# Performance work log

Measured on AMD Instinct MI355X. Metric: run time of the kernel, lower is better.

Reference implementation:

```python
import jax, jax.numpy as jnp
import numpy as np

TS = 6      # texture cube size (hard-coded in module)
S = 256     # image size (NMR default / ref image size)
DIST = 2.732


def _look_at(verts, eye):
    # NMR look_at: camera at eye, looking at origin, up=(0,1,0)
    eye = jnp.asarray(eye, verts.dtype)
    z = -eye / jnp.linalg.norm(eye)
    up = jnp.array([0.0, 1.0, 0.0], verts.dtype)
    x = jnp.cross(up, z)
    x = x / jnp.linalg.norm(x)
    y = jnp.cross(z, x)
    R = jnp.stack([x, y, z])          # rows = camera axes
    return (verts - eye) @ R.T


def _render(verts, faces, tex_flat, eye):
    # verts [V,3], faces [F,3] int, tex_flat [F*TS^3, 3] (tanh already applied)
    v = _look_at(verts, eye)
    fv = v[faces]                      # [F,3,3]
    p0, p1, p2 = fv[:, 0], fv[:, 1], fv[:, 2]
    ps = (2.0 * jnp.arange(S, dtype=verts.dtype) + 1.0 - S) / S
    PX = jnp.broadcast_to(ps[None, :], (S, S)).reshape(-1)      # x right
    PY = jnp.broadcast_to(-ps[:, None], (S, S)).reshape(-1)     # y up (row 0 = top)

    def edge(a, b):
        # signed edge function, [F,HW]
        return ((PX[None, :] - a[:, 0:1]) * (b[:, 1:2] - a[:, 1:2])
                - (PY[None, :] - a[:, 1:2]) * (b[:, 0:1] - a[:, 0:1]))

    e0 = edge(p1, p2)
    e1 = edge(p2, p0)
    e2 = edge(p0, p1)
    # per-face signed area (double area) [F,1]
    area = ((p1[:, 0] - p0[:, 0]) * (p2[:, 1] - p0[:, 1])
            - (p1[:, 1] - p0[:, 1]) * (p2[:, 0] - p0[:, 0]))[:, None]
    ok = jnp.abs(area) > 1e-8
    inv = jnp.where(ok, 1.0 / jnp.where(ok, area, 1.0), 0.0)
    w0, w1, w2 = e0 * inv, e1 * inv, e2 * inv            # barycentric weights
    inside = (w0 >= 0) & (w1 >= 0) & (w2 >= 0) & ok       # both windings (fill_back)
    z = w0 * p0[:, 2:3] + w1 * p1[:, 2:3] + w2 * p2[:, 2:3]
    depth = jnp.where(inside & (z > 0), z, jnp.inf)       # z-buffer candidates
    best = jnp.argmin(depth, axis=0)                      # [HW] winning face
    hit = jnp.take_along_axis(depth, best[None, :], axis=0)[0] < jnp.inf
    wb = jnp.stack([jnp.take_along_axis(w, best[None, :], axis=0)[0]
                    for w in (w0, w1, w2)], axis=-1)       # [HW,3]
    ti = jnp.clip(jnp.round(wb * (TS - 1)), 0, TS - 1).astype(jnp.int32)
    flat = ((best * TS + ti[:, 0]) * TS + ti[:, 1]) * TS + ti[:, 2]
    colors = tex_flat[flat]                                # [HW,3] gather
    img = jnp.where(hit[:, None], colors, 0.0)
    return img.reshape(S, S, 3).transpose(2, 0, 1)[None]   # [1,3,S,S]


def setup_inputs() -> dict:
    key = jax.random.key(0)
    k1, k2, k3, k4, k5 = jax.random.split(key, 5)
    V, F = 252, 500
    return {
        "vertices": jax.random.normal(k1, (1, V, 3), jnp.float32),
        "faces": jax.random.randint(k2, (1, F, 3), 0, V, jnp.int64),
        "textures": jax.random.normal(k3, (1, F, TS, TS, TS, 3), jnp.float32),
        "image_ref": jax.random.uniform(k4, (1, 3, S, S), jnp.float32),
        "image_ref_2": jax.random.uniform(k5, (1, 3, S, S), jnp.float32),
    }


def reference(vertices, faces, textures, image_ref, image_ref_2):
    tex_flat = jnp.tanh(textures[0]).reshape(-1, 3)
    v, f = vertices[0], faces[0]
    # eye = get_points_from_angles(2.732, 180, 0) -> (0, 0, +d)
    img1 = _render(v, f, tex_flat, jnp.array([0.0, 0.0, DIST], jnp.float32))
    loss_one_side = jnp.sum((img1 - image_ref) ** 2)
    # eye = get_points_from_angles(2.732, 0, 0) -> (0, 0, -d)
    img2 = _render(v, f, tex_flat, jnp.array([0.0, 0.0, -DIST], jnp.float32))
    loss_symmetric = jnp.sum((img2 - image_ref_2) ** 2)
    return (loss_one_side + loss_symmetric) / 2
```

## Files before the change

kernel.cpp:

```cpp
#include <hip/hip_runtime.h>
#include <math.h>

#define IMG_S 256
#define NPIX (IMG_S * IMG_S)
#define NFACE 500
#define NCHUNK 8
#define FPC 64
#define PPT 8
#define TSZ 6
#define DIST 2.732f

struct FaceCoef {
    float A0, B0, C0, A1, B1, C1, A2, B2, C2, Az, Bz, Cz;
};

__device__ __forceinline__ void edge_coef(float ax, float ay, float bx, float by,
                                          float inv, float& A, float& B, float& C) {
    float dy = by - ay;
    float dx = bx - ax;
    A = dy * inv;
    B = -dx * inv;
    C = (ay * dx - ax * dy) * inv;
}

__device__ __forceinline__ bool compute_face_bbox(const float* __restrict__ verts,
                                                  const int* __restrict__ faces,
                                                  int f, int view, FaceCoef& fc,
                                                  float& ymin, float& ymax, float& zmax) {
    int i0 = faces[f * 3 + 0];
    int i1 = faces[f * 3 + 1];
    int i2 = faces[f * 3 + 2];

    float v0x = verts[i0 * 3 + 0], v0y = verts[i0 * 3 + 1], v0z = verts[i0 * 3 + 2];
    float v1x = verts[i1 * 3 + 0], v1y = verts[i1 * 3 + 1], v1z = verts[i1 * 3 + 2];
    float v2x = verts[i2 * 3 + 0], v2y = verts[i2 * 3 + 1], v2z = verts[i2 * 3 + 2];

    float p0x, p0y, p0z, p1x, p1y, p1z, p2x, p2y, p2z;
    if (view == 0) {
        p0x = -v0x; p0y = v0y; p0z = DIST - v0z;
        p1x = -v1x; p1y = v1y; p1z = DIST - v1z;
        p2x = -v2x; p2y = v2y; p2z = DIST - v2z;
    } else {
        p0x = v0x; p0y = v0y; p0z = v0z + DIST;
        p1x = v1x; p1y = v1y; p1z = v1z + DIST;
        p2x = v2x; p2y = v2y; p2z = v2z + DIST;
    }

    ymin = fminf(p0y, fminf(p1y, p2y));
    ymax = fmaxf(p0y, fmaxf(p1y, p2y));
    zmax = fmaxf(p0z, fmaxf(p1z, p2z));

    float area = (p1x - p0x) * (p2y - p0y) - (p1y - p0y) * (p2x - p0x);
    bool ok = fabsf(area) > 1e-8f;
    if (!ok) return false;

    float inv = 1.0f / area;
    edge_coef(p1x, p1y, p2x, p2y, inv, fc.A0, fc.B0, fc.C0);
    edge_coef(p2x, p2y, p0x, p0y, inv, fc.A1, fc.B1, fc.C1);
    edge_coef(p0x, p0y, p1x, p1y, inv, fc.A2, fc.B2, fc.C2);
    fc.Az = fc.A0 * p0z + fc.A1 * p1z + fc.A2 * p2z;
    fc.Bz = fc.B0 * p0z + fc.B1 * p1z + fc.B2 * p2z;
    fc.Cz = fc.C0 * p0z + fc.C1 * p1z + fc.C2 * p2z;
    return true;
}

__device__ __forceinline__ float pix_x(int ix) {
    return (2.0f * (float)ix + 1.0f - (float)IMG_S) * (1.0f / (float)IMG_S);
}
__device__ __forceinline__ float pix_y(int iy) {
    return -((2.0f * (float)iy + 1.0f - (float)IMG_S) * (1.0f / (float)IMG_S));
}

__global__ __launch_bounds__(256) void raster_chunk_kernel(
    const float* __restrict__ verts,
    const int*   __restrict__ faces,
    unsigned long long* __restrict__ planes,
    float* __restrict__ out)
{
    __shared__ float4 sc[FPC][3];
    __shared__ int    sidx[FPC];
    __shared__ int    scount;

    const int tile  = blockIdx.x;
    const int chunk = blockIdx.y;
    const int view  = blockIdx.z;
    const int fbase = chunk * FPC;

    if (blockIdx.x == 0 && blockIdx.y == 0 && blockIdx.z == 0 && threadIdx.x == 0)
        out[0] = 0.0f;

    const float py_top = pix_y(tile * PPT);
    const float py_bot = pix_y(tile * PPT + PPT - 1);

    if (threadIdx.x < 64) {
        bool keep = false;
        FaceCoef c;
        int fi = fbase + (int)threadIdx.x;
        if (fi < NFACE) {
            float ymin, ymax, zmax;
            bool ok = compute_face_bbox(verts, faces, fi, view, c, ymin, ymax, zmax);
            keep = ok && (ymax >= py_bot) && (ymin <= py_top) && (zmax > 0.0f);
        }
        unsigned long long bal = __ballot(keep);
        int pos = __popcll(bal & ((1ull << (threadIdx.x & 63)) - 1ull));
        if (keep) {
            sc[pos][0] = make_float4(c.A0, c.B0, c.C0, c.A1);
            sc[pos][1] = make_float4(c.B1, c.C1, c.A2, c.B2);
            sc[pos][2] = make_float4(c.C2, c.Az, c.Bz, c.Cz);
            sidx[pos] = fi;
        }
        if (threadIdx.x == 0) scount = (int)__popcll(bal);
    }
    __syncthreads();
    const int cnt = scount;

    const int ix = threadIdx.x;
    const float px = pix_x(ix);
    float py[PPT];
    #pragma unroll
    for (int k = 0; k < PPT; ++k) py[k] = pix_y(tile * PPT + k);

    float bestz[PPT];
    int   bestj[PPT];
    #pragma unroll
    for (int k = 0; k < PPT; ++k) { bestz[k] = INFINITY; bestj[k] = -1; }

    for (int j = 0; j < cnt; ++j) {
        float4 q0 = sc[j][0];
        float4 q1 = sc[j][1];
        float4 q2 = sc[j][2];
        float d0 = fmaf(px, q0.x, q0.z);
        float d1 = fmaf(px, q0.w, q1.y);
        float d2 = fmaf(px, q1.z, q2.x);
        float dz = fmaf(px, q2.y, q2.w);
        #pragma unroll
        for (int k = 0; k < PPT; ++k) {
            float w0 = fmaf(q0.y, py[k], d0);
            float w1 = fmaf(q1.x, py[k], d1);
            float w2 = fmaf(q1.w, py[k], d2);
            float z  = fmaf(q2.z, py[k], dz);
            float wmin = fminf(w0, fminf(w1, w2));
            float s = fminf(z, bestz[k] - z);
            bool cc = (wmin >= 0.0f) && (s > 0.0f);
            bestz[k] = cc ? z : bestz[k];
            bestj[k] = cc ? j : bestj[k];
        }
    }

    unsigned long long* __restrict__ outp =
        planes + (size_t)(view * NCHUNK + chunk) * NPIX + tile * (PPT * IMG_S) + ix;
    #pragma unroll
    for (int k = 0; k < PPT; ++k) {
        unsigned long long packed = ~0ull;
        if (bestj[k] >= 0)
            packed = ((unsigned long long)__float_as_uint(bestz[k]) << 32) |
                     (unsigned int)sidx[bestj[k]];
        outp[k * IMG_S] = packed;
    }
}

__global__ __launch_bounds__(256) void shade_loss_kernel(
    const float* __restrict__ verts,
    const int*   __restrict__ faces,
    const float* __restrict__ tex,
    const float* __restrict__ ref0,
    const float* __restrict__ ref1,
    const unsigned long long* __restrict__ planes,
    float* __restrict__ out)
{
    __shared__ float red[4];
    const int gid  = blockIdx.x * blockDim.x + threadIdx.x;
    const int view = gid >> 16;
    const int pix  = gid & (NPIX - 1);

    const unsigned long long* p = planes + (size_t)view * NCHUNK * NPIX + pix;
    unsigned long long best = p[0];
    #pragma unroll
    for (int c = 1; c < NCHUNK; ++c) {
        unsigned long long v = p[(size_t)c * NPIX];
        best = (v < best) ? v : best;
    }

    float c0 = 0.0f, c1 = 0.0f, c2 = 0.0f;
    if (best != ~0ull) {
        int fidx = (int)(best & 0xFFFFFFFFu);
        FaceCoef fcw;
        float ymin, ymax, zmax;
        compute_face_bbox(verts, faces, fidx, view, fcw, ymin, ymax, zmax);
        const float px = pix_x(pix & (IMG_S - 1));
        const float py = pix_y(pix >> 8);
        float w0 = fmaf(fcw.B0, py, fmaf(px, fcw.A0, fcw.C0));
        float w1 = fmaf(fcw.B1, py, fmaf(px, fcw.A1, fcw.C1));
        float w2 = fmaf(fcw.B2, py, fmaf(px, fcw.A2, fcw.C2));
        int t0 = (int)fminf(fmaxf(rintf(w0 * (float)(TSZ - 1)), 0.0f), (float)(TSZ - 1));
        int t1 = (int)fminf(fmaxf(rintf(w1 * (float)(TSZ - 1)), 0.0f), (float)(TSZ - 1));
        int t2 = (int)fminf(fmaxf(rintf(w2 * (float)(TSZ - 1)), 0.0f), (float)(TSZ - 1));
        int flat = ((fidx * TSZ + t0) * TSZ + t1) * TSZ + t2;
        const float* t = tex + (long)flat * 3;
        c0 = tanhf(t[0]);
        c1 = tanhf(t[1]);
        c2 = tanhf(t[2]);
    }

    const float* __restrict__ ref = (view == 0) ? ref0 : ref1;
    float d0 = c0 - ref[0 * NPIX + pix];
    float d1 = c1 - ref[1 * NPIX + pix];
    float d2 = c2 - ref[2 * NPIX + pix];
    float acc = fmaf(d0, d0, fmaf(d1, d1, d2 * d2));

    for (int off = 32; off > 0; off >>= 1)
        acc += __shfl_down(acc, off, 64);
    int lane = threadIdx.x & 63;
    int wid = threadIdx.x >> 6;
    if (lane == 0) red[wid] = acc;
    __syncthreads();
    if (threadIdx.x == 0)
        atomicAdd(out, 0.5f * (red[0] + red[1] + red[2] + red[3]));
}

extern "C" void kernel_launch(void* const* d_in, const int* in_sizes, int n_in,
                              void* d_out, int out_size, void* d_ws, size_t ws_size,
                              hipStream_t stream) {
    const float* verts = (const float*)d_in[0];
    const int*   faces = (const int*)d_in[1];
    const float* tex   = (const float*)d_in[2];
    const float* ref0  = (const float*)d_in[3];
    const float* ref1  = (const float*)d_in[4];
    float* out = (float*)d_out;

    unsigned long long* planes = (unsigned long long*)d_ws;

    dim3 grid1(NPIX / (256 * PPT), NCHUNK, 2);
    raster_chunk_kernel<<<grid1, 256, 0, stream>>>(verts, faces, planes, out);

    const int shade_blocks = (2 * NPIX) / 256;
    shade_loss_kernel<<<shade_blocks, 256, 0, stream>>>(verts, faces, tex, ref0, ref1,
                                                        planes, out);
}
```

Baseline: 88.95 us.

## Pack depth and face index into a double and min-reduce with fmin

The raster loop now packs depth bits and face index into a single double and keeps the nearest hit with one fmin, replacing the separate compare, select and index-tracking of the old z-buffer. Faces are also split into two groups. Faces whose vertices all sit in front of the camera skip the per-pixel z>0 test, and only the rest keep it. This trims ALU work in the inner loop, but relies on positive float bit patterns ordering the same as doubles and on double-precision fmin throughput.

Result: no change. 90.54 us (+1.8%).

```diff
diff --git a/kernel.cpp b/kernel.cpp
--- a/kernel.cpp
+++ b/kernel.cpp
@@ -9,6 +9,7 @@
 #define PPT 8
 #define TSZ 6
 #define DIST 2.732f
+#define MISS 0x7FF0000000000000ull
 
 struct FaceCoef {
     float A0, B0, C0, A1, B1, C1, A2, B2, C2, Az, Bz, Cz;
@@ -26,7 +27,8 @@
 __device__ __forceinline__ bool compute_face_bbox(const float* __restrict__ verts,
                                                   const int* __restrict__ faces,
                                                   int f, int view, FaceCoef& fc,
-                                                  float& ymin, float& ymax, float& zmax) {
+                                                  float& ymin, float& ymax,
+                                                  float& zmin, float& zmax) {
     int i0 = faces[f * 3 + 0];
     int i1 = faces[f * 3 + 1];
     int i2 = faces[f * 3 + 2];
@@ -48,6 +50,7 @@
 
     ymin = fminf(p0y, fminf(p1y, p2y));
     ymax = fmaxf(p0y, fmaxf(p1y, p2y));
+    zmin = fminf(p0z, fminf(p1z, p2z));
     zmax = fmaxf(p0z, fmaxf(p1z, p2z));
 
     float area = (p1x - p0x) * (p2y - p0y) - (p1y - p0y) * (p2x - p0x);
@@ -79,7 +82,7 @@
 {
     __shared__ float4 sc[FPC][3];
     __shared__ int    sidx[FPC];
-    __shared__ int    scount;
+    __shared__ int    scnt[2];
 
     const int tile  = blockIdx.x;
     const int chunk = blockIdx.y;
@@ -93,26 +96,33 @@
     const float py_bot = pix_y(tile * PPT + PPT - 1);
 
     if (threadIdx.x < 64) {
-        bool keep = false;
+        bool good = false, bad = false;
         FaceCoef c;
         int fi = fbase + (int)threadIdx.x;
         if (fi < NFACE) {
-            float ymin, ymax, zmax;
-            bool ok = compute_face_bbox(verts, faces, fi, view, c, ymin, ymax, zmax);
-            keep = ok && (ymax >= py_bot) && (ymin <= py_top) && (zmax > 0.0f);
-        }
-        unsigned long long bal = __ballot(keep);
-        int pos = __popcll(bal & ((1ull << (threadIdx.x & 63)) - 1ull));
-        if (keep) {
+            float ymin, ymax, zmin, zmax;
+            bool ok = compute_face_bbox(verts, faces, fi, view, c, ymin, ymax, zmin, zmax);
+            bool hit = ok && (ymax >= py_bot) && (ymin <= py_top) && (zmax > 0.0f);
+            good = hit && (zmin > 1e-3f);
+            bad  = hit && !good;
+        }
+        unsigned long long lmask = (1ull << (threadIdx.x & 63)) - 1ull;
+        unsigned long long bg = __ballot(good);
+        unsigned long long bb = __ballot(bad);
+        int ng = (int)__popcll(bg);
+        int pos = good ? (int)__popcll(bg & lmask)
+                       : ng + (int)__popcll(bb & lmask);
+        if (good || bad) {
             sc[pos][0] = make_float4(c.A0, c.B0, c.C0, c.A1);
             sc[pos][1] = make_float4(c.B1, c.C1, c.A2, c.B2);
             sc[pos][2] = make_float4(c.C2, c.Az, c.Bz, c.Cz);
             sidx[pos] = fi;
         }
-        if (threadIdx.x == 0) scount = (int)__popcll(bal);
+        if (threadIdx.x == 0) { scnt[0] = ng; scnt[1] = ng + (int)__popcll(bb); }
     }
     __syncthreads();
-    const int cnt = scount;
+    const int ng  = scnt[0];
+    const int cnt = scnt[1];
 
     const int ix = threadIdx.x;
     const float px = pix_x(ix);
@@ -120,15 +130,15 @@
     #pragma unroll
     for (int k = 0; k < PPT; ++k) py[k] = pix_y(tile * PPT + k);
 
-    float bestz[PPT];
-    int   bestj[PPT];
-    #pragma unroll
-    for (int k = 0; k < PPT; ++k) { bestz[k] = INFINITY; bestj[k] = -1; }
-
-    for (int j = 0; j < cnt; ++j) {
+    double best[PPT];
+    #pragma unroll
+    for (int k = 0; k < PPT; ++k) best[k] = __hiloint2double(0x7FF00000, 0);
+
+    for (int j = 0; j < ng; ++j) {
         float4 q0 = sc[j][0];
         float4 q1 = sc[j][1];
         float4 q2 = sc[j][2];
+        int idx = sidx[j];
         float d0 = fmaf(px, q0.x, q0.z);
         float d1 = fmaf(px, q0.w, q1.y);
         float d2 = fmaf(px, q1.z, q2.x);
@@ -139,24 +149,40 @@
             float w1 = fmaf(q1.x, py[k], d1);
             float w2 = fmaf(q1.w, py[k], d2);
             float z  = fmaf(q2.z, py[k], dz);
-            float wmin = fminf(w0, fminf(w1, w2));
-            float s = fminf(z, bestz[k] - z);
-            bool cc = (wmin >= 0.0f) && (s > 0.0f);
-            bestz[k] = cc ? z : bestz[k];
-            bestj[k] = cc ? j : bestj[k];
+            bool cc = fminf(w0, fminf(w1, w2)) >= 0.0f;
+            double cand = __hiloint2double(cc ? __float_as_int(z) : 0x7FF00000,
+                                           cc ? idx : 0);
+            best[k] = fmin(best[k], cand);
+        }
+    }
+
+    for (int j = ng; j < cnt; ++j) {
+        float4 q0 = sc[j][0];
+        float4 q1 = sc[j][1];
+        float4 q2 = sc[j][2];
+        int idx = sidx[j];
+        float d0 = fmaf(px, q0.x, q0.z);
+        float d1 = fmaf(px, q0.w, q1.y);
+        float d2 = fmaf(px, q1.z, q2.x);
+        float dz = fmaf(px, q2.y, q2.w);
+        #pragma unroll
+        for (int k = 0; k < PPT; ++k) {
+            float w0 = fmaf(q0.y, py[k], d0);
+            float w1 = fmaf(q1.x, py[k], d1);
+            float w2 = fmaf(q1.w, py[k], d2);
+            float z  = fmaf(q2.z, py[k], dz);
+            bool cc = (fminf(w0, fminf(w1, w2)) >= 0.0f) && (z > 0.0f);
+            double cand = __hiloint2double(cc ? __float_as_int(z) : 0x7FF00000,
+                                           cc ? idx : 0);
+            best[k] = fmin(best[k], cand);
         }
     }
 
     unsigned long long* __restrict__ outp =
         planes + (size_t)(view * NCHUNK + chunk) * NPIX + tile * (PPT * IMG_S) + ix;
     #pragma unroll
-    for (int k = 0; k < PPT; ++k) {
-        unsigned long long packed = ~0ull;
-        if (bestj[k] >= 0)
-            packed = ((unsigned long long)__float_as_uint(bestz[k]) << 32) |
-                     (unsigned int)sidx[bestj[k]];
-        outp[k * IMG_S] = packed;
-    }
+    for (int k = 0; k < PPT; ++k)
+        outp[k * IMG_S] = __double_as_longlong(best[k]);
 }
 
 __global__ __launch_bounds__(256) void shade_loss_kernel(
@@ -182,11 +208,11 @@
     }
 
     float c0 = 0.0f, c1 = 0.0f, c2 = 0.0f;
-    if (best != ~0ull) {
+    if (best < MISS) {
         int fidx = (int)(best & 0xFFFFFFFFu);
         FaceCoef fcw;
-        float ymin, ymax, zmax;
-        compute_face_bbox(verts, faces, fidx, view, fcw, ymin, ymax, zmax);
+        float ymin, ymax, zmin, zmax;
+        compute_face_bbox(verts, faces, fidx, view, fcw, ymin, ymax, zmin, zmax);
         const float px = pix_x(pix & (IMG_S - 1));
         const float py = pix_y(pix >> 8);
         float w0 = fmaf(fcw.B0, py, fmaf(px, fcw.A0, fcw.C0));
```
